# Performance work log

Hardware: AMD Instinct MI355X
Metric: run time of the kernel (lower is better)

## Reference

```python
import jax, jax.numpy as jnp
import numpy as np

B, SEQ_LEN, CHANNELS, PRED_LEN = 64, 1024, 512, 720
KERNEL = 25
PAD = (KERNEL - 1) // 2  # 12
IN_LEN = SEQ_LEN // 2    # 512
INV_SQRT2 = 1.0 / np.sqrt(2.0).astype(np.float32)


def dct2_ortho_matrix(N):
    # Orthonormal DCT-II basis: X_k = s_k * sum_n x_n cos(pi*(n+0.5)*k/N)
    n = np.arange(N, dtype=np.float64)
    k = np.arange(N, dtype=np.float64)
    M = np.cos(np.pi * (n[None, :] + 0.5) * k[:, None] / N)
    scale = np.sqrt(2.0 / N) * np.ones(N)
    scale[0] = np.sqrt(1.0 / N)
    return jnp.asarray((scale[:, None] * M).astype(np.float32))  # [k, n]


def setup_inputs() -> dict:
    key = jax.random.key(0)
    k1, k2, k3, k4, k5 = jax.random.split(key, 5)
    bound = 1.0 / np.sqrt(IN_LEN)
    return {
        "x": jax.random.normal(k1, (B, SEQ_LEN, CHANNELS), dtype=jnp.float32),
        "W_seasonal": jax.random.uniform(k2, (PRED_LEN, IN_LEN), jnp.float32, -bound, bound),
        "b_seasonal": jax.random.uniform(k3, (PRED_LEN,), jnp.float32, -bound, bound),
        "W_trend": jax.random.uniform(k4, (PRED_LEN, IN_LEN), jnp.float32, -bound, bound),
        "b_trend": jax.random.uniform(k5, (PRED_LEN,), jnp.float32, -bound, bound),
    }


def reference(x, W_seasonal, b_seasonal, W_trend, b_trend):
    # --- series decomposition: moving average (edge-padded, window 25) ---
    padded = jnp.pad(x, ((0, 0), (PAD, PAD), (0, 0)), mode="edge")  # [B, L+24, C]
    cs = jnp.cumsum(padded, axis=1)
    cs = jnp.pad(cs, ((0, 0), (1, 0), (0, 0)))  # leading zero, [B, L+25, C]
    trend = (cs[:, KERNEL:, :] - cs[:, :-KERNEL, :]) / KERNEL  # [B, L, C]
    seasonal = x - trend

    # [B, C, L]
    s = jnp.transpose(seasonal, (0, 2, 1))
    t = jnp.transpose(trend, (0, 2, 1))

    # --- grouped conv1d with [1,1]/sqrt(2), stride 2 (Haar low-pass downsample) ---
    def down(v):
        return (v[..., 0::2] + v[..., 1::2]) * INV_SQRT2  # [B, C, L/2]

    s = down(s)
    t = down(t)

    # --- orthonormal DCT-II over last axis, then divide by length ---
    Mdct = dct2_ortho_matrix(IN_LEN)  # [k, n]
    s = jnp.einsum("bcn,kn->bck", s, Mdct) / IN_LEN
    t = jnp.einsum("bcn,kn->bck", t, Mdct) / IN_LEN

    # --- shared Linear per branch ---
    s_out = jnp.einsum("bck,pk->bcp", s, W_seasonal) + b_seasonal
    t_out = jnp.einsum("bck,pk->bcp", t, W_trend) + b_trend

    out = s_out + t_out  # [B, C, pred_len]
    return jnp.transpose(out, (0, 2, 1))  # [B, pred_len, C]
```

## Files before the change

### kernel.cpp

```cpp
#include <hip/hip_runtime.h>
#include <hip/hip_bf16.h>
#include <math.h>


#define BATCH 64
#define SEQ 1024
#define CH 512
#define PRED 720
#define INV_SQRT2 0.70710678118654752440f

typedef __attribute__((ext_vector_type(4))) float floatx4;
typedef __attribute__((ext_vector_type(8))) short bf16x8;

#define KBF_OFF   0ull
#define BIAS_OFF  1572864ull
#define MW_OFF    1575936ull
#define WEFFS_OFF 2624512ull
#define WEFFT_OFF 4099072ull
#define XT_OFF    5573632ull
#define WS_NEED   (XT_OFF + 67108864ull)

__global__ void build_M(float* __restrict__ Mw) {
    int idx = blockIdx.x * 256 + threadIdx.x;
    int k = idx >> 9, n = idx & 511;
    int m = ((2 * n + 1) * k) & 2047;
    float ang = (float)m * (float)(M_PI / 1024.0);
    float scale = (k == 0) ? 0.04419417382415922f
                           : 0.0625f;
    Mw[idx] = cosf(ang) * scale * (1.0f / 512.0f);
}

__global__ void build_weff(const float* __restrict__ Ws_in, const float* __restrict__ Wt_in,
                           const float* __restrict__ Mw,
                           float* __restrict__ outS, float* __restrict__ outT) {
    const float* W = blockIdx.z ? Wt_in : Ws_in;
    float* out     = blockIdx.z ? outT  : outS;
    int n0 = blockIdx.x * 64;
    int p0 = blockIdx.y * 16;
    int t  = threadIdx.x;
    int tn = t & 63, tp = t >> 6;
    int pbase = p0 + tp * 4;
    __shared__ float wt[16][512];
    __shared__ float mt[64][64];
#pragma unroll
    for (int i = 0; i < 8; i++) {
        int q = i * 256 + t;
        int r = q >> 7, kq4 = q & 127;
        floatx4 v = *reinterpret_cast<const floatx4*>(&W[(size_t)(p0 + r) * 512 + kq4 * 4]);
        *reinterpret_cast<floatx4*>(&wt[r][kq4 * 4]) = v;
    }
    float a0 = 0.f, a1 = 0.f, a2 = 0.f, a3 = 0.f;
    for (int kb = 0; kb < 512; kb += 64) {
        __syncthreads();
        for (int i = 0; i < 16; i++) {
            int idx = t + i * 256;
            mt[idx >> 6][idx & 63] = Mw[(size_t)(kb + (idx >> 6)) * 512 + n0 + (idx & 63)];
        }
        __syncthreads();
        for (int kk = 0; kk < 64; kk++) {
            float m = mt[kk][tn];
            int kg = kb + kk;
            a0 += wt[tp * 4 + 0][kg] * m;
            a1 += wt[tp * 4 + 1][kg] * m;
            a2 += wt[tp * 4 + 2][kg] * m;
            a3 += wt[tp * 4 + 3][kg] * m;
        }
    }
    out[(size_t)(pbase + 0) * 512 + n0 + tn] = a0;
    out[(size_t)(pbase + 1) * 512 + n0 + tn] = a1;
    out[(size_t)(pbase + 2) * 512 + n0 + tn] = a2;
    out[(size_t)(pbase + 3) * 512 + n0 + tn] = a3;
}

__device__ __forceinline__ int tcnt(int j, int l) {
    if (l == 0)    return max(0, 13 - j);
    if (l == 1023) return max(0, j - 1010);
    int d = l - j; if (d < 0) d = -d;
    return (d <= 12) ? 1 : 0;
}

__global__ void build_kmat(const float* __restrict__ Ws, const float* __restrict__ Wt,
                           const float* __restrict__ bs, const float* __restrict__ bt,
                           __hip_bfloat16* __restrict__ Kbf, float* __restrict__ bias) {
    int idx = blockIdx.x * 256 + threadIdx.x;
    int p = idx >> 10, l = idx & 1023;
    if (p >= PRED) { Kbf[idx] = __float2bfloat16(0.0f); return; }
    if (l == 0) bias[p] = bs[p] + bt[p];
    float v = INV_SQRT2 * Ws[(size_t)p * 512 + (l >> 1)];
    int jlo = max(0, l - 12), jhi = min(1023, l + 12);
    float acc = 0.f;
    for (int n = (jlo >> 1); n <= (jhi >> 1); n++) {
        int c = tcnt(2 * n, l) + tcnt(2 * n + 1, l);
        if (c) acc += (Wt[(size_t)p * 512 + n] - Ws[(size_t)p * 512 + n]) * (float)c;
    }
    v += acc * (INV_SQRT2 / 25.0f);
    Kbf[idx] = __float2bfloat16(v);
}

__device__ __forceinline__ void async_ld16(const void* g, void* l) {
    __builtin_amdgcn_global_load_lds((const __attribute__((address_space(1))) void*)g,
                                     (__attribute__((address_space(3))) void*)l, 16, 0, 0);
}

__device__ __forceinline__ short f2bf(float f) {
    __hip_bfloat16 h = __float2bfloat16(f);
    return *reinterpret_cast<short*>(&h);
}

__global__ void __launch_bounds__(256) xpose(const float* __restrict__ x,
                                             short* __restrict__ xT) {
    __shared__ float lds[64][65];
    int t = threadIdx.x;
    int l0 = blockIdx.x * 64, c0 = blockIdx.y * 64, b = blockIdx.z;
    const float* xb = x + (size_t)b * SEQ * CH;
    int row4 = t >> 4, cq = t & 15;
#pragma unroll
    for (int i = 0; i < 4; i++) {
        int row = row4 + i * 16;
        floatx4 v = *reinterpret_cast<const floatx4*>(
            xb + (size_t)(l0 + row) * CH + c0 + cq * 4);
#pragma unroll
        for (int e = 0; e < 4; e++) lds[row][cq * 4 + e] = v[e];
    }
    __syncthreads();
    size_t outb = (size_t)b * CH * SEQ;
#pragma unroll
    for (int r = 0; r < 2; r++) {
        int u = r * 256 + t;
        int lr = u & 7, c = u >> 3;
        bf16x8 s;
#pragma unroll
        for (int e = 0; e < 8; e++) s[e] = f2bf(lds[lr * 8 + e][c]);
        *reinterpret_cast<bf16x8*>(&xT[outb + (size_t)(c0 + c) * SEQ + l0 + lr * 8]) = s;
    }
}

__global__ void __launch_bounds__(256) gemm_main_t(
    const short* __restrict__ Kbf, const short* __restrict__ xT,
    const float* __restrict__ bias, float* __restrict__ out) {
    __shared__ __align__(16) short ldsA[128 * 32];
    int t = threadIdx.x;
    int wave = t >> 6, lane = t & 63;
    int bid = blockIdx.x;
    int work = (bid & 7) * 192 + (bid >> 3);
    int mt = work % 6;
    int grp = work / 6;
    int nt = grp & 3, b = grp >> 2;
    int wm = wave >> 1, wn = wave & 1;
    int lm = lane & 15, kq = lane >> 4;
    const short* Ag = Kbf + (size_t)mt * 128 * 1024;
    const short* xrow[4];
#pragma unroll
    for (int j = 0; j < 4; j++) {
        int c = nt * 128 + wn * 64 + j * 16 + lm;
        xrow[j] = xT + ((size_t)b * CH + c) * 1024 + kq * 8;
    }

    floatx4 acc[4][4];
#pragma unroll
    for (int i = 0; i < 4; i++)
#pragma unroll
        for (int j = 0; j < 4; j++)
            acc[i][j] = (floatx4){0.f, 0.f, 0.f, 0.f};

    for (int k0 = 0; k0 < 1024; k0 += 32) {
#pragma unroll
        for (int rdi = 0; rdi < 2; rdi++) {
            int q = rdi * 256 + t;
            int row = ((q >> 6) << 4) + (q & 15);
            int ko = ((q >> 4) & 3) * 8;
            async_ld16(Ag + (size_t)row * 1024 + k0 + ko,
                       (char*)ldsA + rdi * 4096 + wave * 1024);
        }
        bf16x8 bfrag[4];
#pragma unroll
        for (int j = 0; j < 4; j++)
            bfrag[j] = *reinterpret_cast<const bf16x8*>(xrow[j] + k0);
        __syncthreads();
        bf16x8 af[4];
#pragma unroll
        for (int i = 0; i < 4; i++)
            af[i] = *reinterpret_cast<const bf16x8*>(
                (const char*)ldsA + ((wm * 4 + i) << 10) + (lane << 4));
#pragma unroll
        for (int i = 0; i < 4; i++)
#pragma unroll
            for (int j = 0; j < 4; j++)
                acc[i][j] = __builtin_amdgcn_mfma_f32_16x16x32_bf16(af[i], bfrag[j], acc[i][j], 0, 0, 0);
        __syncthreads();
    }

    int p0r = mt * 128 + wm * 64;
    int cb = nt * 128 + wn * 64 + lm;
    size_t outb = (size_t)b * PRED * CH;
#pragma unroll
    for (int i = 0; i < 4; i++) {
#pragma unroll
        for (int r = 0; r < 4; r++) {
            int p = p0r + i * 16 + kq * 4 + r;
            if (p < PRED) {
                float bv = bias[p];
#pragma unroll
                for (int j = 0; j < 4; j++)
                    __builtin_nontemporal_store(acc[i][j][r] + bv,
                                                &out[outb + (size_t)p * CH + cb + j * 16]);
            }
        }
    }
}

__global__ void __launch_bounds__(256) gemm_main(
    const short* __restrict__ Kbf, const float* __restrict__ x,
    const float* __restrict__ bias, float* __restrict__ out) {
    __shared__ __align__(16) short ldsA[128 * 32];
    int t = threadIdx.x;
    int wave = t >> 6, lane = t & 63;
    int mt = blockIdx.x % 6, nt = blockIdx.x / 6;
    int b  = blockIdx.y;
    int wm = wave >> 1, wn = wave & 1;
    const short* Ag = Kbf + (size_t)mt * 128 * 1024;
    const float* xb = x + (size_t)b * SEQ * CH;
    int lm = lane & 15, kq = lane >> 4;
    int cj[4];
    for (int j = 0; j < 4; j++) cj[j] = nt * 128 + wn * 64 + j * 16 + lm;

    floatx4 acc[4][4];
    for (int i = 0; i < 4; i++)
        for (int j = 0; j < 4; j++)
            acc[i][j] = (floatx4){0.f, 0.f, 0.f, 0.f};

    for (int k0 = 0; k0 < 1024; k0 += 32) {
        for (int rdi = 0; rdi < 2; rdi++) {
            int q = rdi * 256 + t;
            int row = q >> 2, ko = (q & 3) * 8;
            async_ld16(Ag + (size_t)row * 1024 + k0 + ko,
                       (char*)ldsA + rdi * 4096 + wave * 1024);
        }
        bf16x8 bfrag[4];
        int krow = k0 + kq * 8;
#pragma unroll
        for (int j = 0; j < 4; j++) {
            const float* xc = xb + (size_t)krow * CH + cj[j];
            bf16x8 bv;
#pragma unroll
            for (int i = 0; i < 8; i++) bv[i] = f2bf(xc[(size_t)i * CH]);
            bfrag[j] = bv;
        }
        __syncthreads();
        bf16x8 af[4];
        for (int i = 0; i < 4; i++)
            af[i] = *(const bf16x8*)&ldsA[(wm * 64 + i * 16 + lm) * 32 + kq * 8];
        for (int i = 0; i < 4; i++)
            for (int j = 0; j < 4; j++)
                acc[i][j] = __builtin_amdgcn_mfma_f32_16x16x32_bf16(af[i], bfrag[j], acc[i][j], 0, 0, 0);
        __syncthreads();
    }

    int p0 = mt * 128 + wm * 64;
    size_t outb = (size_t)b * PRED * CH;
    for (int i = 0; i < 4; i++) {
        for (int r = 0; r < 4; r++) {
            int p = p0 + i * 16 + kq * 4 + r;
            if (p < PRED) {
                float bv = bias[p];
                for (int j = 0; j < 4; j++) {
                    out[outb + (size_t)p * CH + cj[j]] = acc[i][j][r] + bv;
                }
            }
        }
    }
}

extern "C" void kernel_launch(void* const* d_in, const int* in_sizes, int n_in,
                              void* d_out, int out_size, void* d_ws, size_t ws_size,
                              hipStream_t stream) {
    const float* xp = nullptr; const float* wp[2] = {nullptr, nullptr};
    const float* bp[2] = {nullptr, nullptr};
    int wn = 0, bn = 0;
    for (int i = 0; i < n_in; i++) {
        if (in_sizes[i] == 33554432) xp = (const float*)d_in[i];
        else if (in_sizes[i] == 368640 && wn < 2) wp[wn++] = (const float*)d_in[i];
        else if (in_sizes[i] == 720 && bn < 2) bp[bn++] = (const float*)d_in[i];
    }
    if (!xp || wn != 2 || bn != 2) {
        xp = (const float*)d_in[0]; wp[0] = (const float*)d_in[1];
        bp[0] = (const float*)d_in[2]; wp[1] = (const float*)d_in[3];
        bp[1] = (const float*)d_in[4];
    }
    float* out = (float*)d_out;

    char* ws = (char*)d_ws;
    __hip_bfloat16* Kbf = (__hip_bfloat16*)(ws + KBF_OFF);
    float* bias  = (float*)(ws + BIAS_OFF);
    float* Mw    = (float*)(ws + MW_OFF);
    float* WeffS = (float*)(ws + WEFFS_OFF);
    float* WeffT = (float*)(ws + WEFFT_OFF);
    short* xT    = (short*)(ws + XT_OFF);

    bool big = (ws_size >= (size_t)WS_NEED);

    if (big) xpose<<<dim3(16, 8, 64), 256, 0, stream>>>(xp, xT);
    build_M<<<1024, 256, 0, stream>>>(Mw);
    build_weff<<<dim3(8, 45, 2), 256, 0, stream>>>(wp[0], wp[1], Mw, WeffS, WeffT);
    build_kmat<<<3072, 256, 0, stream>>>(WeffS, WeffT, bp[0], bp[1], Kbf, bias);
    if (big)
        gemm_main_t<<<1536, 256, 0, stream>>>((const short*)Kbf, (const short*)xT, bias, out);
    else
        gemm_main<<<dim3(24, 64), 256, 0, stream>>>((const short*)Kbf, xp, bias, out);
}
```

Baseline: 407.8 us.

## Double-buffer A and B tiles in LDS for main GEMM; retile weight fold

The main bf16 GEMM now stages both the kernel-matrix tile and the transposed-input tile into LDS through async loads, with two buffers so the next k-step loads while the current one runs MFMAs. This cuts the barriers per iteration from two to one, and B fragments come from LDS instead of direct global loads. The small build_weff kernel is rewritten as a 64x64 register-tiled SGEMM with 4x4 outputs per thread, giving fewer blocks and more reuse. LDS use per block grows fourfold, which may limit occupancy despite the launch-bounds hint.

Result: faster. 379.3 us (-7.0%).

```diff
diff --git a/kernel.cpp b/kernel.cpp
--- a/kernel.cpp
+++ b/kernel.cpp
@@ -30,46 +30,54 @@
     Mw[idx] = cosf(ang) * scale * (1.0f / 512.0f);
 }
 
-__global__ void build_weff(const float* __restrict__ Ws_in, const float* __restrict__ Wt_in,
-                           const float* __restrict__ Mw,
-                           float* __restrict__ outS, float* __restrict__ outT) {
+__global__ void __launch_bounds__(256) build_weff(
+    const float* __restrict__ Ws_in, const float* __restrict__ Wt_in,
+    const float* __restrict__ Mw,
+    float* __restrict__ outS, float* __restrict__ outT) {
     const float* W = blockIdx.z ? Wt_in : Ws_in;
     float* out     = blockIdx.z ? outT  : outS;
     int n0 = blockIdx.x * 64;
-    int p0 = blockIdx.y * 16;
+    int p0 = blockIdx.y * 64;
     int t  = threadIdx.x;
-    int tn = t & 63, tp = t >> 6;
-    int pbase = p0 + tp * 4;
-    __shared__ float wt[16][512];
-    __shared__ float mt[64][64];
-#pragma unroll
-    for (int i = 0; i < 8; i++) {
-        int q = i * 256 + t;
-        int r = q >> 7, kq4 = q & 127;
-        floatx4 v = *reinterpret_cast<const floatx4*>(&W[(size_t)(p0 + r) * 512 + kq4 * 4]);
-        *reinterpret_cast<floatx4*>(&wt[r][kq4 * 4]) = v;
-    }
-    float a0 = 0.f, a1 = 0.f, a2 = 0.f, a3 = 0.f;
-    for (int kb = 0; kb < 512; kb += 64) {
-        __syncthreads();
-        for (int i = 0; i < 16; i++) {
-            int idx = t + i * 256;
-            mt[idx >> 6][idx & 63] = Mw[(size_t)(kb + (idx >> 6)) * 512 + n0 + (idx & 63)];
-        }
-        __syncthreads();
-        for (int kk = 0; kk < 64; kk++) {
-            float m = mt[kk][tn];
-            int kg = kb + kk;
-            a0 += wt[tp * 4 + 0][kg] * m;
-            a1 += wt[tp * 4 + 1][kg] * m;
-            a2 += wt[tp * 4 + 2][kg] * m;
-            a3 += wt[tp * 4 + 3][kg] * m;
-        }
-    }
-    out[(size_t)(pbase + 0) * 512 + n0 + tn] = a0;
-    out[(size_t)(pbase + 1) * 512 + n0 + tn] = a1;
-    out[(size_t)(pbase + 2) * 512 + n0 + tn] = a2;
-    out[(size_t)(pbase + 3) * 512 + n0 + tn] = a3;
+    int tx = t & 15, ty = t >> 4;
+    __shared__ float wlds[32][65];
+    __shared__ float mlds[32][64];
+    float a[4][4] = {};
+    for (int kb = 0; kb < 512; kb += 32) {
+        __syncthreads();
+        {
+            int pp = t >> 2, kk0 = (t & 3) * 8;
+            int prow = min(p0 + pp, PRED - 1);
+            const float* wsrc = &W[(size_t)prow * 512 + kb + kk0];
+#pragma unroll
+            for (int e = 0; e < 8; e++) wlds[kk0 + e][pp] = wsrc[e];
+        }
+        {
+            int kk = t >> 3, nn = (t & 7) * 8;
+            const float* msrc = &Mw[(size_t)(kb + kk) * 512 + n0 + nn];
+            *reinterpret_cast<floatx4*>(&mlds[kk][nn])     = *reinterpret_cast<const floatx4*>(&msrc[0]);
+            *reinterpret_cast<floatx4*>(&mlds[kk][nn + 4]) = *reinterpret_cast<const floatx4*>(&msrc[4]);
+        }
+        __syncthreads();
+#pragma unroll
+        for (int kk = 0; kk < 32; kk++) {
+            floatx4 wv = *reinterpret_cast<const floatx4*>(&wlds[kk][ty * 4]);
+            floatx4 mv = *reinterpret_cast<const floatx4*>(&mlds[kk][tx * 4]);
+#pragma unroll
+            for (int i = 0; i < 4; i++)
+#pragma unroll
+                for (int j = 0; j < 4; j++)
+                    a[i][j] += wv[i] * mv[j];
+        }
+    }
+#pragma unroll
+    for (int i = 0; i < 4; i++) {
+        int p = p0 + ty * 4 + i;
+        if (p < PRED) {
+            floatx4 v = {a[i][0], a[i][1], a[i][2], a[i][3]};
+            *reinterpret_cast<floatx4*>(&out[(size_t)p * 512 + n0 + tx * 4]) = v;
+        }
+    }
 }
 
 __device__ __forceinline__ int tcnt(int j, int l) {
@@ -135,10 +143,10 @@
     }
 }
 
-__global__ void __launch_bounds__(256) gemm_main_t(
+__global__ void __launch_bounds__(256, 4) gemm_main_t(
     const short* __restrict__ Kbf, const short* __restrict__ xT,
     const float* __restrict__ bias, float* __restrict__ out) {
-    __shared__ __align__(16) short ldsA[128 * 32];
+    __shared__ __align__(16) short ldsbuf[2 * 2 * 128 * 32];
     int t = threadIdx.x;
     int wave = t >> 6, lane = t & 63;
     int bid = blockIdx.x;
@@ -147,13 +155,16 @@
     int grp = work / 6;
     int nt = grp & 3, b = grp >> 2;
     int wm = wave >> 1, wn = wave & 1;
-    int lm = lane & 15, kq = lane >> 4;
     const short* Ag = Kbf + (size_t)mt * 128 * 1024;
-    const short* xrow[4];
-#pragma unroll
-    for (int j = 0; j < 4; j++) {
-        int c = nt * 128 + wn * 64 + j * 16 + lm;
-        xrow[j] = xT + ((size_t)b * CH + c) * 1024 + kq * 8;
+    const short* Bg = xT + ((size_t)b * CH + nt * 128) * 1024;
+
+    size_t srcoff[2];
+#pragma unroll
+    for (int rdi = 0; rdi < 2; rdi++) {
+        int q = rdi * 256 + t;
+        int row = ((q >> 6) << 4) + (q & 15);
+        int ko = ((q >> 4) & 3) * 8;
+        srcoff[rdi] = (size_t)row * 1024 + ko;
     }
 
     floatx4 acc[4][4];
@@ -163,35 +174,46 @@
         for (int j = 0; j < 4; j++)
             acc[i][j] = (floatx4){0.f, 0.f, 0.f, 0.f};
 
-    for (int k0 = 0; k0 < 1024; k0 += 32) {
-#pragma unroll
-        for (int rdi = 0; rdi < 2; rdi++) {
-            int q = rdi * 256 + t;
-            int row = ((q >> 6) << 4) + (q & 15);
-            int ko = ((q >> 4) & 3) * 8;
-            async_ld16(Ag + (size_t)row * 1024 + k0 + ko,
-                       (char*)ldsA + rdi * 4096 + wave * 1024);
-        }
-        bf16x8 bfrag[4];
+#pragma unroll
+    for (int rdi = 0; rdi < 2; rdi++) {
+        char* dA = (char*)ldsbuf + rdi * 4096 + wave * 1024;
+        async_ld16(Ag + srcoff[rdi], dA);
+        async_ld16(Bg + srcoff[rdi], dA + 8192);
+    }
+    __syncthreads();
+
+    int cur = 0;
+    for (int it = 0; it < 32; ++it) {
+        if (it < 31) {
+            int k0n = (it + 1) * 32;
+            char* base = (char*)ldsbuf + (cur ^ 1) * 16384;
+#pragma unroll
+            for (int rdi = 0; rdi < 2; rdi++) {
+                char* dA = base + rdi * 4096 + wave * 1024;
+                async_ld16(Ag + srcoff[rdi] + k0n, dA);
+                async_ld16(Bg + srcoff[rdi] + k0n, dA + 8192);
+            }
+        }
+        const char* cb = (const char*)ldsbuf + cur * 16384;
+        bf16x8 af[4], bf[4];
+#pragma unroll
+        for (int i = 0; i < 4; i++)
+            af[i] = *reinterpret_cast<const bf16x8*>(cb + ((wm * 4 + i) << 10) + (lane << 4));
 #pragma unroll
         for (int j = 0; j < 4; j++)
-            bfrag[j] = *reinterpret_cast<const bf16x8*>(xrow[j] + k0);
-        __syncthreads();
-        bf16x8 af[4];
+            bf[j] = *reinterpret_cast<const bf16x8*>(cb + 8192 + ((wn * 4 + j) << 10) + (lane << 4));
 #pragma unroll
         for (int i = 0; i < 4; i++)
-            af[i] = *reinterpret_cast<const bf16x8*>(
-                (const char*)ldsA + ((wm * 4 + i) << 10) + (lane << 4));
-#pragma unroll
-        for (int i = 0; i < 4; i++)
 #pragma unroll
             for (int j = 0; j < 4; j++)
-                acc[i][j] = __builtin_amdgcn_mfma_f32_16x16x32_bf16(af[i], bfrag[j], acc[i][j], 0, 0, 0);
-        __syncthreads();
-    }
-
+                acc[i][j] = __builtin_amdgcn_mfma_f32_16x16x32_bf16(af[i], bf[j], acc[i][j], 0, 0, 0);
+        __syncthreads();
+        cur ^= 1;
+    }
+
+    int lm = lane & 15, kq = lane >> 4;
     int p0r = mt * 128 + wm * 64;
-    int cb = nt * 128 + wn * 64 + lm;
+    int cb2 = nt * 128 + wn * 64 + lm;
     size_t outb = (size_t)b * PRED * CH;
 #pragma unroll
     for (int i = 0; i < 4; i++) {
@@ -203,7 +225,7 @@
 #pragma unroll
                 for (int j = 0; j < 4; j++)
                     __builtin_nontemporal_store(acc[i][j][r] + bv,
-                                                &out[outb + (size_t)p * CH + cb + j * 16]);
+                                                &out[outb + (size_t)p * CH + cb2 + j * 16]);
             }
         }
     }
@@ -301,7 +323,7 @@
 
     if (big) xpose<<<dim3(16, 8, 64), 256, 0, stream>>>(xp, xT);
     build_M<<<1024, 256, 0, stream>>>(Mw);
-    build_weff<<<dim3(8, 45, 2), 256, 0, stream>>>(wp[0], wp[1], Mw, WeffS, WeffT);
+    build_weff<<<dim3(8, 12, 2), 256, 0, stream>>>(wp[0], wp[1], Mw, WeffS, WeffT);
     build_kmat<<<3072, 256, 0, stream>>>(WeffS, WeffT, bp[0], bp[1], Kbf, bias);
     if (big)
         gemm_main_t<<<1536, 256, 0, stream>>>((const short*)Kbf, (const short*)xT, bias, out);
```
